# Kernel tuning notes

Hardware: AMD Instinct MI355X
Metric: run time of the kernel (lower is better)

Reference implementation:

```python
import jax, jax.numpy as jnp
import numpy as np

LUT_SIZE = 65536
OUT_F = 4096
IN_F = 4096
B, S = 4, 2048


def setup_inputs() -> dict:
    key = jax.random.key(0)
    k_x, k_idx, k_lut = jax.random.split(key, 3)
    x = jax.random.normal(k_x, (B, S, IN_F), dtype=jnp.float32)
    grid_indices = jax.random.randint(k_idx, (OUT_F, IN_F), 0, LUT_SIZE, dtype=jnp.int32)
    lut = jax.random.normal(k_lut, (LUT_SIZE,), dtype=jnp.float32)
    scale = jnp.ones((OUT_F, 1), dtype=jnp.float32)
    return {"x": x, "grid_indices": grid_indices, "lut": lut, "scale": scale}


def reference(x, grid_indices, lut, scale):
    # Dequantize: LUT gather per weight element, per-output-row scale.
    weights = lut[grid_indices] * scale  # [out_f, in_f]
    # F.linear(x, weights) == x @ weights.T
    return jnp.einsum('bsi,oi->bso', x, weights)
```

## Files before the change

### kernel.cpp

```cpp
#include <hip/hip_runtime.h>
#include <hip/hip_bf16.h>


typedef __bf16 bf16x8 __attribute__((ext_vector_type(8)));
typedef float f32x16 __attribute__((ext_vector_type(16)));

#define AS1(p) ((__attribute__((address_space(1))) void*)(p))
#define AS3(p) ((__attribute__((address_space(3))) void*)(p))

static constexpr int M_DIM = 8192;
static constexpr int N_DIM = 4096;
static constexpr int K_DIM = 4096;

__global__ __launch_bounds__(1024) void dequant_w_kernel(
    const int* __restrict__ idx, const float* __restrict__ lut,
    int4* __restrict__ wout) {
  __shared__ unsigned short lut_s[32768];
  const int tid = threadIdx.x;
  const int4* i4 = (const int4*)idx;
  const float4* lut4 = (const float4*)lut;

  int4 ia[4], ib[4];
  union { unsigned short u[8]; int4 q; } o[4];
#pragma unroll
  for (int it = 0; it < 4; ++it) {
    const int w = blockIdx.x * 4096 + it * 1024 + tid;
    ia[it] = i4[2 * w];
    ib[it] = i4[2 * w + 1];
  }

#pragma unroll
  for (int i8 = 0; i8 < 8; ++i8) {
    const int c = i8 * 1024 + tid;
    const float4 f = lut4[c];
    union { unsigned short u[4]; unsigned long long q; } s;
    __bf16 b0 = (__bf16)f.x, b1 = (__bf16)f.y, b2 = (__bf16)f.z, b3 = (__bf16)f.w;
    s.u[0] = *(const unsigned short*)&b0;
    s.u[1] = *(const unsigned short*)&b1;
    s.u[2] = *(const unsigned short*)&b2;
    s.u[3] = *(const unsigned short*)&b3;
    *(unsigned long long*)&lut_s[4 * c] = s.q;
  }
  __syncthreads();
#pragma unroll
  for (int it = 0; it < 4; ++it) {
    if (ia[it].x < 32768) o[it].u[0] = lut_s[ia[it].x];
    if (ia[it].y < 32768) o[it].u[1] = lut_s[ia[it].y];
    if (ia[it].z < 32768) o[it].u[2] = lut_s[ia[it].z];
    if (ia[it].w < 32768) o[it].u[3] = lut_s[ia[it].w];
    if (ib[it].x < 32768) o[it].u[4] = lut_s[ib[it].x];
    if (ib[it].y < 32768) o[it].u[5] = lut_s[ib[it].y];
    if (ib[it].z < 32768) o[it].u[6] = lut_s[ib[it].z];
    if (ib[it].w < 32768) o[it].u[7] = lut_s[ib[it].w];
  }
  __syncthreads();

#pragma unroll
  for (int i8 = 0; i8 < 8; ++i8) {
    const int c = i8 * 1024 + tid;
    const float4 f = lut4[8192 + c];
    union { unsigned short u[4]; unsigned long long q; } s;
    __bf16 b0 = (__bf16)f.x, b1 = (__bf16)f.y, b2 = (__bf16)f.z, b3 = (__bf16)f.w;
    s.u[0] = *(const unsigned short*)&b0;
    s.u[1] = *(const unsigned short*)&b1;
    s.u[2] = *(const unsigned short*)&b2;
    s.u[3] = *(const unsigned short*)&b3;
    *(unsigned long long*)&lut_s[4 * c] = s.q;
  }
  __syncthreads();
#pragma unroll
  for (int it = 0; it < 4; ++it) {
    if (ia[it].x >= 32768) o[it].u[0] = lut_s[ia[it].x - 32768];
    if (ia[it].y >= 32768) o[it].u[1] = lut_s[ia[it].y - 32768];
    if (ia[it].z >= 32768) o[it].u[2] = lut_s[ia[it].z - 32768];
    if (ia[it].w >= 32768) o[it].u[3] = lut_s[ia[it].w - 32768];
    if (ib[it].x >= 32768) o[it].u[4] = lut_s[ib[it].x - 32768];
    if (ib[it].y >= 32768) o[it].u[5] = lut_s[ib[it].y - 32768];
    if (ib[it].z >= 32768) o[it].u[6] = lut_s[ib[it].z - 32768];
    if (ib[it].w >= 32768) o[it].u[7] = lut_s[ib[it].w - 32768];
    const int w = blockIdx.x * 4096 + it * 1024 + tid;
    wout[w] = o[it].q;
  }
}

__global__ __launch_bounds__(256) void cvt_x_kernel(
    const float4* __restrict__ x, int4* __restrict__ aout) {
  const int t = blockIdx.x * 256 + threadIdx.x;
  const float4 a = x[2 * t];
  const float4 b = x[2 * t + 1];
  union { bf16x8 v; int4 q; } u;
  u.v[0] = (__bf16)a.x;  u.v[1] = (__bf16)a.y;
  u.v[2] = (__bf16)a.z;  u.v[3] = (__bf16)a.w;
  u.v[4] = (__bf16)b.x;  u.v[5] = (__bf16)b.y;
  u.v[6] = (__bf16)b.z;  u.v[7] = (__bf16)b.w;
  aout[t] = u.q;
}


__device__ __forceinline__ void load_af(bf16x8 af[2][4], const char* p,
                                        const int ck[4]) {
#pragma unroll
  for (int il = 0; il < 2; ++il)
#pragma unroll
    for (int t = 0; t < 4; ++t)
      af[il][t] = *(const bf16x8*)(p + il * 4096 + ck[t]);
}

__device__ __forceinline__ void load_bf(bf16x8 bf[4], const char* p,
                                        const int ck[4]) {
#pragma unroll
  for (int t = 0; t < 4; ++t)
    bf[t] = *(const bf16x8*)(p + ck[t]);
}

template <int HB, int J>
__device__ __forceinline__ void mma_quad(f32x16 acc[4][2],
                                         const bf16x8 af[2][4],
                                         const bf16x8 bf[4]) {
#pragma unroll
  for (int t = 0; t < 4; ++t)
#pragma unroll
    for (int il = 0; il < 2; ++il)
      acc[HB * 2 + il][J] = __builtin_amdgcn_mfma_f32_32x32x16_bf16(
          af[il][t], bf[t], acc[HB * 2 + il][J], 0, 0, 0);
}

#define BAR __builtin_amdgcn_s_barrier()
#define VMCNT4 asm volatile("s_waitcnt vmcnt(4)" ::: "memory")
#define LGKM0                                          \
  do {                                                 \
    asm volatile("s_waitcnt lgkmcnt(0)" ::: "memory"); \
    __builtin_amdgcn_sched_barrier(0);                 \
  } while (0)

#define ldsA(PI, HB) (lds + (PI) * 32768 + (HB) * 16384 + aBase)
#define ldsB(PI, JH) (lds + 65536 + (PI) * 32768 + (JH) * 16384 + bBase)

#define STAGE_A(PI, HB, KN)                                                    \
  do {                                                                         \
    const size_t gofs = gA0 + (size_t)(HB)*524288 + (size_t)(KN)*2;            \
    __builtin_amdgcn_global_load_lds(                                          \
        AS1(Ag + gofs),                                                        \
        AS3(lds + (PI)*32768 + (HB)*16384 + tid * 16), 16, 0, 0);              \
    __builtin_amdgcn_global_load_lds(                                          \
        AS1(Ag + gofs + 1048576),                                              \
        AS3(lds + (PI)*32768 + (HB)*16384 + 8192 + tid * 16), 16, 0, 0);       \
  } while (0)

#define STAGE_B(PI, HB, KN)                                                    \
  do {                                                                         \
    const size_t gofs = gB0 + (size_t)(HB)*262144 + (size_t)(KN)*2;            \
    __builtin_amdgcn_global_load_lds(                                          \
        AS1(Bg + gofs),                                                        \
        AS3(lds + 65536 + (PI)*32768 + (HB)*16384 + tid * 16), 16, 0, 0);      \
    __builtin_amdgcn_global_load_lds(                                          \
        AS1(Bg + gofs + 1048576),                                              \
        AS3(lds + 65536 + (PI)*32768 + (HB)*16384 + 8192 + tid * 16), 16, 0,   \
        0);                                                                    \
  } while (0)

#define TILE(PI, KN)                        \
  do {                                      \
                                    \
    load_af(af, ldsA(PI, 0), ck);           \
    load_bf(bf, ldsB(PI, 0), ck);           \
    STAGE_A((PI) ^ 1, 0, KN);               \
    BAR;                                    \
    LGKM0;                                  \
    __builtin_amdgcn_s_setprio(1);          \
    mma_quad<0, 0>(acc, af, bf);            \
    __builtin_amdgcn_s_setprio(0);          \
    VMCNT4;                                 \
    BAR;                                    \
                                    \
    load_bf(bf, ldsB(PI, 1), ck);           \
    STAGE_B((PI) ^ 1, 0, KN);               \
    BAR;                                    \
    LGKM0;                                  \
    __builtin_amdgcn_s_setprio(1);          \
    mma_quad<0, 1>(acc, af, bf);            \
    __builtin_amdgcn_s_setprio(0);          \
    VMCNT4;                                 \
    BAR;                                    \
                                    \
    load_af(af, ldsA(PI, 1), ck);           \
    STAGE_B((PI) ^ 1, 1, KN);               \
    BAR;                                    \
    LGKM0;                                  \
    __builtin_amdgcn_s_setprio(1);          \
    mma_quad<1, 1>(acc, af, bf);            \
    __builtin_amdgcn_s_setprio(0);          \
    BAR;                                    \
                                    \
    load_bf(bf, ldsB(PI, 0), ck);           \
    STAGE_A((PI) ^ 1, 1, KN);               \
    BAR;                                    \
    LGKM0;                                  \
    __builtin_amdgcn_s_setprio(1);          \
    mma_quad<1, 0>(acc, af, bf);            \
    __builtin_amdgcn_s_setprio(0);          \
    VMCNT4;                                 \
    BAR;                                    \
  } while (0)

__global__ __launch_bounds__(512) void gemm8_kernel(
    const unsigned short* __restrict__ A, const unsigned short* __restrict__ Bw,
    const float* __restrict__ scale, float* __restrict__ C) {
  extern __shared__ __align__(16) char lds[];

  const int tid = threadIdx.x;
  const int lane = tid & 63;
  const int lm = lane & 31;
  const int lh = lane >> 5;
  const int wave = tid >> 6;
  const int wr = wave >> 2;
  const int wc = wave & 3;

  int wg = blockIdx.x;
  wg = ((wg & 7) << 6) | (wg >> 3);
  const int bx = wg & 15;
  const int by = wg >> 4;
  const size_t m_blk = (size_t)by * 256;
  const size_t n_blk = (size_t)bx * 256;

  const char* Ag = (const char*)(A + m_blk * K_DIM);
  const char* Bg = (const char*)(Bw + n_blk * K_DIM);

  const int u = tid >> 3;
  const int cs = (tid & 7) ^ (u & 7);
  const size_t gA0 = (size_t)u * 8192 + (size_t)cs * 16;
  const size_t gB0 = (size_t)((u & 31) + ((u >> 5) << 6)) * 8192 +
                     (size_t)cs * 16;

  const int aBase = (lm + 64 * wr) * 128;
  const int bBase = (lm + 32 * wc) * 128;
  int ck[4];
#pragma unroll
  for (int t = 0; t < 4; ++t) ck[t] = (((2 * t + lh) ^ (lm & 7)) << 4);

  f32x16 acc[4][2] = {};
  bf16x8 af[2][4];
  bf16x8 bf[4];

  STAGE_A(0, 0, 0);
  STAGE_B(0, 0, 0);
  STAGE_B(0, 1, 0);
  STAGE_A(0, 1, 0);
  VMCNT4;
  BAR;

  for (int it = 0; it < 32; ++it) {
    const int kb = it << 7;
    TILE(0, kb + 64);
    TILE(1, (kb + 128) & 4095);
  }

  const float sc0 = scale[n_blk + wc * 64 + lm];
  const float sc1 = scale[n_blk + wc * 64 + 32 + lm];
#pragma unroll
  for (int i = 0; i < 4; ++i) {
    const size_t mb = m_blk + wr * 128 + i * 32 + 4 * lh;
#pragma unroll
    for (int g = 0; g < 4; ++g) {
#pragma unroll
      for (int rr = 0; rr < 4; ++rr) {
        const size_t m = mb + 8 * g + rr;
        float* Crow = C + m * N_DIM + n_blk + wc * 64 + lm;
        Crow[0]  = acc[i][0][g * 4 + rr] * sc0;
        Crow[32] = acc[i][1][g * 4 + rr] * sc1;
      }
    }
  }
}

extern "C" void kernel_launch(void* const* d_in, const int* in_sizes, int n_in,
                              void* d_out, int out_size, void* d_ws, size_t ws_size,
                              hipStream_t stream) {
  const float* x     = (const float*)d_in[0];
  const int*   gidx  = (const int*)d_in[1];
  const float* lut   = (const float*)d_in[2];
  const float* scale = (const float*)d_in[3];
  float* out = (float*)d_out;

  unsigned short* wbf = (unsigned short*)d_ws;
  unsigned short* abf = wbf + (size_t)N_DIM * K_DIM;

  dequant_w_kernel<<<dim3(512), dim3(1024), 0, stream>>>(gidx, lut, (int4*)wbf);
  cvt_x_kernel<<<dim3((M_DIM * (size_t)K_DIM) / 8 / 256), dim3(256), 0, stream>>>(
      (const float4*)x, (int4*)abf);
  gemm8_kernel<<<dim3(512), dim3(512), 131072, stream>>>(abf, wbf, scale, out);
}
```

Baseline: 523.2 us.

## Switch GEMM to 16x16x32 MFMA tiles and single-pass full-LUT dequant

The GEMM moves from 32x32x16 to 16x16x32 bf16 MFMA, with a new LDS layout and swizzle, a new warp-to-subtile mapping and a new epilogue. The dequant kernel now holds the whole 64K-entry bf16 LUT in 128 KB of dynamic LDS, replacing the two-pass half-LUT scheme and its extra barriers. The MFMA change is meant to alter LDS read patterns and register pressure. The larger LDS footprint limits dequant occupancy to one block per CU, and the launch_bounds(512,2) hint conflicts with the 128 KB GEMM LDS allocation.

```diff
diff --git a/kernel.cpp b/kernel.cpp
--- a/kernel.cpp
+++ b/kernel.cpp
@@ -3,7 +3,7 @@
 
 
 typedef __bf16 bf16x8 __attribute__((ext_vector_type(8)));
-typedef float f32x16 __attribute__((ext_vector_type(16)));
+typedef float f32x4 __attribute__((ext_vector_type(4)));
 
 #define AS1(p) ((__attribute__((address_space(1))) void*)(p))
 #define AS3(p) ((__attribute__((address_space(3))) void*)(p))
@@ -15,23 +15,15 @@
 __global__ __launch_bounds__(1024) void dequant_w_kernel(
     const int* __restrict__ idx, const float* __restrict__ lut,
     int4* __restrict__ wout) {
-  __shared__ unsigned short lut_s[32768];
+  extern __shared__ __align__(16) char smem[];
+  unsigned short* lut_s = (unsigned short*)smem;
   const int tid = threadIdx.x;
   const int4* i4 = (const int4*)idx;
   const float4* lut4 = (const float4*)lut;
 
-  int4 ia[4], ib[4];
-  union { unsigned short u[8]; int4 q; } o[4];
-#pragma unroll
-  for (int it = 0; it < 4; ++it) {
-    const int w = blockIdx.x * 4096 + it * 1024 + tid;
-    ia[it] = i4[2 * w];
-    ib[it] = i4[2 * w + 1];
-  }
-
-#pragma unroll
-  for (int i8 = 0; i8 < 8; ++i8) {
-    const int c = i8 * 1024 + tid;
+#pragma unroll
+  for (int i = 0; i < 16; ++i) {
+    const int c = i * 1024 + tid;
     const float4 f = lut4[c];
     union { unsigned short u[4]; unsigned long long q; } s;
     __bf16 b0 = (__bf16)f.x, b1 = (__bf16)f.y, b2 = (__bf16)f.z, b3 = (__bf16)f.w;
@@ -42,44 +34,18 @@
     *(unsigned long long*)&lut_s[4 * c] = s.q;
   }
   __syncthreads();
+
 #pragma unroll
   for (int it = 0; it < 4; ++it) {
-    if (ia[it].x < 32768) o[it].u[0] = lut_s[ia[it].x];
-    if (ia[it].y < 32768) o[it].u[1] = lut_s[ia[it].y];
-    if (ia[it].z < 32768) o[it].u[2] = lut_s[ia[it].z];
-    if (ia[it].w < 32768) o[it].u[3] = lut_s[ia[it].w];
-    if (ib[it].x < 32768) o[it].u[4] = lut_s[ib[it].x];
-    if (ib[it].y < 32768) o[it].u[5] = lut_s[ib[it].y];
-    if (ib[it].z < 32768) o[it].u[6] = lut_s[ib[it].z];
-    if (ib[it].w < 32768) o[it].u[7] = lut_s[ib[it].w];
-  }
-  __syncthreads();
-
-#pragma unroll
-  for (int i8 = 0; i8 < 8; ++i8) {
-    const int c = i8 * 1024 + tid;
-    const float4 f = lut4[8192 + c];
-    union { unsigned short u[4]; unsigned long long q; } s;
-    __bf16 b0 = (__bf16)f.x, b1 = (__bf16)f.y, b2 = (__bf16)f.z, b3 = (__bf16)f.w;
-    s.u[0] = *(const unsigned short*)&b0;
-    s.u[1] = *(const unsigned short*)&b1;
-    s.u[2] = *(const unsigned short*)&b2;
-    s.u[3] = *(const unsigned short*)&b3;
-    *(unsigned long long*)&lut_s[4 * c] = s.q;
-  }
-  __syncthreads();
-#pragma unroll
-  for (int it = 0; it < 4; ++it) {
-    if (ia[it].x >= 32768) o[it].u[0] = lut_s[ia[it].x - 32768];
-    if (ia[it].y >= 32768) o[it].u[1] = lut_s[ia[it].y - 32768];
-    if (ia[it].z >= 32768) o[it].u[2] = lut_s[ia[it].z - 32768];
-    if (ia[it].w >= 32768) o[it].u[3] = lut_s[ia[it].w - 32768];
-    if (ib[it].x >= 32768) o[it].u[4] = lut_s[ib[it].x - 32768];
-    if (ib[it].y >= 32768) o[it].u[5] = lut_s[ib[it].y - 32768];
-    if (ib[it].z >= 32768) o[it].u[6] = lut_s[ib[it].z - 32768];
-    if (ib[it].w >= 32768) o[it].u[7] = lut_s[ib[it].w - 32768];
     const int w = blockIdx.x * 4096 + it * 1024 + tid;
-    wout[w] = o[it].q;
+    const int4 a = i4[2 * w];
+    const int4 b = i4[2 * w + 1];
+    union { unsigned short u[8]; int4 q; } o;
+    o.u[0] = lut_s[a.x]; o.u[1] = lut_s[a.y];
+    o.u[2] = lut_s[a.z]; o.u[3] = lut_s[a.w];
+    o.u[4] = lut_s[b.x]; o.u[5] = lut_s[b.y];
+    o.u[6] = lut_s[b.z]; o.u[7] = lut_s[b.w];
+    wout[w] = o.q;
   }
 }
 
@@ -97,32 +63,32 @@
 }
 
 
-__device__ __forceinline__ void load_af(bf16x8 af[2][4], const char* p,
-                                        const int ck[4]) {
-#pragma unroll
-  for (int il = 0; il < 2; ++il)
-#pragma unroll
-    for (int t = 0; t < 4; ++t)
-      af[il][t] = *(const bf16x8*)(p + il * 4096 + ck[t]);
-}
-
-__device__ __forceinline__ void load_bf(bf16x8 bf[4], const char* p,
-                                        const int ck[4]) {
-#pragma unroll
-  for (int t = 0; t < 4; ++t)
-    bf[t] = *(const bf16x8*)(p + ck[t]);
-}
-
-template <int HB, int J>
-__device__ __forceinline__ void mma_quad(f32x16 acc[4][2],
-                                         const bf16x8 af[2][4],
-                                         const bf16x8 bf[4]) {
-#pragma unroll
-  for (int t = 0; t < 4; ++t)
-#pragma unroll
-    for (int il = 0; il < 2; ++il)
-      acc[HB * 2 + il][J] = __builtin_amdgcn_mfma_f32_32x32x16_bf16(
-          af[il][t], bf[t], acc[HB * 2 + il][J], 0, 0, 0);
+__device__ __forceinline__ void ld_a(bf16x8 af[4][2], const char* p) {
+#pragma unroll
+  for (int i = 0; i < 4; ++i)
+#pragma unroll
+    for (int s = 0; s < 2; ++s)
+      af[i][s] = *(const bf16x8*)(p + i * 2048 + s * 64);
+}
+
+__device__ __forceinline__ void ld_b(bf16x8 bf[2][2], const char* p) {
+#pragma unroll
+  for (int j = 0; j < 2; ++j)
+#pragma unroll
+    for (int s = 0; s < 2; ++s)
+      bf[j][s] = *(const bf16x8*)(p + j * 2048 + s * 64);
+}
+
+__device__ __forceinline__ void quad(f32x4 acc[4][2], const bf16x8 af[4][2],
+                                     const bf16x8 bf[2][2]) {
+#pragma unroll
+  for (int s = 0; s < 2; ++s)
+#pragma unroll
+    for (int i = 0; i < 4; ++i)
+#pragma unroll
+      for (int j = 0; j < 2; ++j)
+        acc[i][j] = __builtin_amdgcn_mfma_f32_16x16x32_bf16(
+            af[i][s], bf[j][s], acc[i][j], 0, 0, 0);
 }
 
 #define BAR __builtin_amdgcn_s_barrier()
@@ -133,85 +99,84 @@
     __builtin_amdgcn_sched_barrier(0);                 \
   } while (0)
 
-#define ldsA(PI, HB) (lds + (PI) * 32768 + (HB) * 16384 + aBase)
-#define ldsB(PI, JH) (lds + 65536 + (PI) * 32768 + (JH) * 16384 + bBase)
-
-#define STAGE_A(PI, HB, KN)                                                    \
+#define ldsA(PI, H) (lds + (PI) * 32768 + (H) * 16384 + aRd)
+#define ldsB(PI, H) (lds + 65536 + (PI) * 32768 + (H) * 16384 + bRd)
+
+#define STAGE_A(PI, H, KN)                                                     \
   do {                                                                         \
-    const size_t gofs = gA0 + (size_t)(HB)*524288 + (size_t)(KN)*2;            \
-    __builtin_amdgcn_global_load_lds(                                          \
-        AS1(Ag + gofs),                                                        \
-        AS3(lds + (PI)*32768 + (HB)*16384 + tid * 16), 16, 0, 0);              \
-    __builtin_amdgcn_global_load_lds(                                          \
-        AS1(Ag + gofs + 1048576),                                              \
-        AS3(lds + (PI)*32768 + (HB)*16384 + 8192 + tid * 16), 16, 0, 0);       \
-  } while (0)
-
-#define STAGE_B(PI, HB, KN)                                                    \
+    const size_t so = sOfs + (size_t)(H) * 1048576 + (size_t)(KN) * 2;         \
+    __builtin_amdgcn_global_load_lds(                                          \
+        AS1(Ag + so), AS3(lds + (PI) * 32768 + (H) * 16384 + sDst), 16, 0, 0); \
+    __builtin_amdgcn_global_load_lds(                                          \
+        AS1(Ag + so + 524288),                                                 \
+        AS3(lds + (PI) * 32768 + (H) * 16384 + 8192 + sDst), 16, 0, 0);        \
+  } while (0)
+
+#define STAGE_B(PI, H, KN)                                                     \
   do {                                                                         \
-    const size_t gofs = gB0 + (size_t)(HB)*262144 + (size_t)(KN)*2;            \
-    __builtin_amdgcn_global_load_lds(                                          \
-        AS1(Bg + gofs),                                                        \
-        AS3(lds + 65536 + (PI)*32768 + (HB)*16384 + tid * 16), 16, 0, 0);      \
-    __builtin_amdgcn_global_load_lds(                                          \
-        AS1(Bg + gofs + 1048576),                                              \
-        AS3(lds + 65536 + (PI)*32768 + (HB)*16384 + 8192 + tid * 16), 16, 0,   \
+    const size_t so = sOfs + (size_t)(H) * 1048576 + (size_t)(KN) * 2;         \
+    __builtin_amdgcn_global_load_lds(                                          \
+        AS1(Bg + so), AS3(lds + 65536 + (PI) * 32768 + (H) * 16384 + sDst),    \
+        16, 0, 0);                                                             \
+    __builtin_amdgcn_global_load_lds(                                          \
+        AS1(Bg + so + 524288),                                                 \
+        AS3(lds + 65536 + (PI) * 32768 + (H) * 16384 + 8192 + sDst), 16, 0,    \
         0);                                                                    \
   } while (0)
 
-#define TILE(PI, KN)                        \
-  do {                                      \
-                                    \
-    load_af(af, ldsA(PI, 0), ck);           \
-    load_bf(bf, ldsB(PI, 0), ck);           \
-    STAGE_A((PI) ^ 1, 0, KN);               \
-    BAR;                                    \
-    LGKM0;                                  \
-    __builtin_amdgcn_s_setprio(1);          \
-    mma_quad<0, 0>(acc, af, bf);            \
-    __builtin_amdgcn_s_setprio(0);          \
-    VMCNT4;                                 \
-    BAR;                                    \
-                                    \
-    load_bf(bf, ldsB(PI, 1), ck);           \
-    STAGE_B((PI) ^ 1, 0, KN);               \
-    BAR;                                    \
-    LGKM0;                                  \
-    __builtin_amdgcn_s_setprio(1);          \
-    mma_quad<0, 1>(acc, af, bf);            \
-    __builtin_amdgcn_s_setprio(0);          \
-    VMCNT4;                                 \
-    BAR;                                    \
-                                    \
-    load_af(af, ldsA(PI, 1), ck);           \
-    STAGE_B((PI) ^ 1, 1, KN);               \
-    BAR;                                    \
-    LGKM0;                                  \
-    __builtin_amdgcn_s_setprio(1);          \
-    mma_quad<1, 1>(acc, af, bf);            \
-    __builtin_amdgcn_s_setprio(0);          \
-    BAR;                                    \
-                                    \
-    load_bf(bf, ldsB(PI, 0), ck);           \
-    STAGE_A((PI) ^ 1, 1, KN);               \
-    BAR;                                    \
-    LGKM0;                                  \
-    __builtin_amdgcn_s_setprio(1);          \
-    mma_quad<1, 0>(acc, af, bf);            \
-    __builtin_amdgcn_s_setprio(0);          \
-    VMCNT4;                                 \
-    BAR;                                    \
-  } while (0)
-
-__global__ __launch_bounds__(512) void gemm8_kernel(
+#define TILE(PI, KN)                   \
+  do {                                 \
+              \
+    ld_a(af, ldsA(PI, 0));             \
+    ld_b(bf0, ldsB(PI, 0));            \
+    STAGE_A((PI) ^ 1, 0, KN);          \
+    BAR;                               \
+    LGKM0;                             \
+    __builtin_amdgcn_s_setprio(1);     \
+    quad(acc[0][0], af, bf0);          \
+    __builtin_amdgcn_s_setprio(0);     \
+    VMCNT4;                            \
+    BAR;                               \
+              \
+    ld_b(bf1, ldsB(PI, 1));            \
+    STAGE_B((PI) ^ 1, 0, KN);          \
+    BAR;                               \
+    LGKM0;                             \
+    __builtin_amdgcn_s_setprio(1);     \
+    quad(acc[0][1], af, bf1);          \
+    __builtin_amdgcn_s_setprio(0);     \
+    VMCNT4;                            \
+    BAR;                               \
+              \
+    ld_a(af, ldsA(PI, 1));             \
+    STAGE_B((PI) ^ 1, 1, KN);          \
+    BAR;                               \
+    LGKM0;                             \
+    __builtin_amdgcn_s_setprio(1);     \
+    quad(acc[1][1], af, bf1);          \
+    __builtin_amdgcn_s_setprio(0);     \
+    BAR;                               \
+    \
+    STAGE_A((PI) ^ 1, 1, KN);          \
+    BAR;                               \
+    __builtin_amdgcn_s_setprio(1);     \
+    quad(acc[1][0], af, bf0);          \
+    __builtin_amdgcn_s_setprio(0);     \
+    VMCNT4;                            \
+    BAR;                               \
+  } while (0)
+
+__global__ __launch_bounds__(512, 2) void gemm16_kernel(
     const unsigned short* __restrict__ A, const unsigned short* __restrict__ Bw,
     const float* __restrict__ scale, float* __restrict__ C) {
-  extern __shared__ __align__(16) char lds[];
+  extern __shared__ __align__(16) char smem[];
+  char* lds = smem;
 
   const int tid = threadIdx.x;
   const int lane = tid & 63;
-  const int lm = lane & 31;
-  const int lh = lane >> 5;
+  const int lt = lane & 15;
+  const int lq = lane >> 4;
+  const int swz = ((lane >> 2) & 1) << 5;
   const int wave = tid >> 6;
   const int wr = wave >> 2;
   const int wc = wave & 3;
@@ -226,21 +191,17 @@
   const char* Ag = (const char*)(A + m_blk * K_DIM);
   const char* Bg = (const char*)(Bw + n_blk * K_DIM);
 
-  const int u = tid >> 3;
-  const int cs = (tid & 7) ^ (u & 7);
-  const size_t gA0 = (size_t)u * 8192 + (size_t)cs * 16;
-  const size_t gB0 = (size_t)((u & 31) + ((u >> 5) << 6)) * 8192 +
-                     (size_t)cs * 16;
-
-  const int aBase = (lm + 64 * wr) * 128;
-  const int bBase = (lm + 32 * wc) * 128;
-  int ck[4];
-#pragma unroll
-  for (int t = 0; t < 4; ++t) ck[t] = (((2 * t + lh) ^ (lm & 7)) << 4);
-
-  f32x16 acc[4][2] = {};
-  bf16x8 af[2][4];
-  bf16x8 bf[4];
+  const int aRd = (64 * wr + lt) * 128 + ((lq << 4) ^ swz);
+  const int bRd = (32 * wc + lt) * 128 + ((lq << 4) ^ swz);
+
+  const int c_log = (tid & 7) ^ ((tid >> 4) & 2);
+  const size_t sOfs = (size_t)(tid >> 3) * 8192 + (size_t)c_log * 16;
+  const int sDst = tid * 16;
+
+  f32x4 acc[2][2][4][2] = {};
+  bf16x8 af[4][2];
+  bf16x8 bf0[2][2];
+  bf16x8 bf1[2][2];
 
   STAGE_A(0, 0, 0);
   STAGE_B(0, 0, 0);
@@ -255,22 +216,27 @@
     TILE(1, (kb + 128) & 4095);
   }
 
-  const float sc0 = scale[n_blk + wc * 64 + lm];
-  const float sc1 = scale[n_blk + wc * 64 + 32 + lm];
-#pragma unroll
-  for (int i = 0; i < 4; ++i) {
-    const size_t mb = m_blk + wr * 128 + i * 32 + 4 * lh;
-#pragma unroll
-    for (int g = 0; g < 4; ++g) {
-#pragma unroll
-      for (int rr = 0; rr < 4; ++rr) {
-        const size_t m = mb + 8 * g + rr;
-        float* Crow = C + m * N_DIM + n_blk + wc * 64 + lm;
-        Crow[0]  = acc[i][0][g * 4 + rr] * sc0;
-        Crow[32] = acc[i][1][g * 4 + rr] * sc1;
+  float scv[2][2];
+#pragma unroll
+  for (int qn = 0; qn < 2; ++qn)
+#pragma unroll
+    for (int j = 0; j < 2; ++j)
+      scv[qn][j] = scale[n_blk + qn * 128 + wc * 32 + j * 16 + lt];
+
+#pragma unroll
+  for (int qm = 0; qm < 2; ++qm)
+#pragma unroll
+    for (int i = 0; i < 4; ++i)
+#pragma unroll
+      for (int r = 0; r < 4; ++r) {
+        const size_t m = m_blk + qm * 128 + wr * 64 + i * 16 + lq * 4 + r;
+        float* Cm = C + m * N_DIM + n_blk + wc * 32 + lt;
+#pragma unroll
+        for (int qn = 0; qn < 2; ++qn)
+#pragma unroll
+          for (int j = 0; j < 2; ++j)
+            Cm[qn * 128 + j * 16] = acc[qm][qn][i][j][r] * scv[qn][j];
       }
-    }
-  }
 }
 
 extern "C" void kernel_launch(void* const* d_in, const int* in_sizes, int n_in,
@@ -285,8 +251,9 @@
   unsigned short* wbf = (unsigned short*)d_ws;
   unsigned short* abf = wbf + (size_t)N_DIM * K_DIM;
 
-  dequant_w_kernel<<<dim3(512), dim3(1024), 0, stream>>>(gidx, lut, (int4*)wbf);
+  dequant_w_kernel<<<dim3(512), dim3(1024), 131072, stream>>>(gidx, lut,
+                                                              (int4*)wbf);
   cvt_x_kernel<<<dim3((M_DIM * (size_t)K_DIM) / 8 / 256), dim3(256), 0, stream>>>(
       (const float4*)x, (int4*)abf);
-  gemm8_kernel<<<dim3(512), dim3(512), 131072, stream>>>(abf, wbf, scale, out);
-}
+  gemm16_kernel<<<dim3(512), dim3(512), 131072, stream>>>(abf, wbf, scale, out);
+}
```

Measured after the change: 499.6 us. -4.5%, faster.
